# Kernel tuning notes

Hardware: AMD Instinct MI355X
Metric: run time of the kernel (lower is better)

The kernel has to match this reference:

```python
import jax, jax.numpy as jnp
import numpy as np

B, C, P, D = 4096, 1000, 10, 256
N = C * P            # total prototypes
E = 160000           # edges among prototypes
MARGIN = -0.1
LOSS_WEIGHT = 0.1
EPS = 1e-12          # F.normalize eps


def _gcn_conv(x, src, dst, deg_isqrt, w, b):
    # PyG GCNConv: symmetric-normalized aggregation with self-loops (added by caller)
    xw = x @ w                                   # [N, D]
    norm = deg_isqrt[src] * deg_isqrt[dst]       # [E+N]
    msg = norm[:, None] * xw[src]                # [E+N, D]
    out = jax.ops.segment_sum(msg, dst, num_segments=N)
    return out + b


def setup_inputs() -> dict:
    key = jax.random.key(0)
    ks = jax.random.split(key, 8)
    return {
        "hidden": jax.random.normal(ks[0], (B, D), jnp.float32),
        "labels": jax.random.randint(ks[1], (B,), 0, C),
        "edge_index": jax.random.randint(ks[2], (2, E), 0, N),
        "node_features": 0.02 * jax.random.normal(ks[3], (N, D), jnp.float32),
        "w1": jax.random.normal(ks[4], (D, D), jnp.float32) / np.sqrt(D),
        "b1": jnp.zeros((D,), jnp.float32),
        "w2": jax.random.normal(ks[5], (D, D), jnp.float32) / np.sqrt(D),
        "b2": jnp.zeros((D,), jnp.float32),
    }


def reference(hidden, labels, edge_index, node_features, w1, b1, w2, b2):
    # --- PrototypeGCN over the prototype graph (self-loops + sym norm) ---
    loops = jnp.arange(N, dtype=edge_index.dtype)
    src = jnp.concatenate([edge_index[0], loops])
    dst = jnp.concatenate([edge_index[1], loops])
    deg = jax.ops.segment_sum(jnp.ones_like(dst, jnp.float32), dst, num_segments=N)
    deg_isqrt = jnp.where(deg > 0, jax.lax.rsqrt(jnp.maximum(deg, 1.0)), 0.0)
    x = node_features
    x = jax.nn.relu(_gcn_conv(x, src, dst, deg_isqrt, w1, b1))
    x = jax.nn.relu(_gcn_conv(x, src, dst, deg_isqrt, w2, b2))

    # --- cosine similarity, per-class max over prototypes ---
    hidden_norm = hidden / jnp.maximum(jnp.linalg.norm(hidden, axis=1, keepdims=True), EPS)
    proto_norm = x / jnp.maximum(jnp.linalg.norm(x, axis=1, keepdims=True), EPS)
    sim = (1.0 + hidden_norm @ proto_norm.T) / 2.0          # [B, N]
    sim_pc = sim.reshape(B, C, P)
    output = sim_pc.max(axis=2)                              # [B, C]
    topk_idx = sim_pc.argmax(axis=2)                         # [B, C]

    # --- margin-masked cross entropy ---
    ar = jnp.arange(B)
    true_scores = output[ar, labels]
    pred_labels = output.argmax(axis=1)
    pred_scores = output.max(axis=1)
    mask = (true_scores - pred_scores) > MARGIN              # [B] bool
    cnt = mask.sum()
    per_ce = -jax.nn.log_softmax(output, axis=1)[ar, labels]
    ce_loss = jnp.sum(per_ce * mask) / jnp.maximum(cnt, 1).astype(per_ce.dtype)

    # dispersion = -mean(proto_norm @ proto_norm.T) = -||sum_i p_i||^2 / N^2
    s = proto_norm.sum(axis=0)
    dispersion_loss = -(s @ s) / (N * N)
    total_loss = jnp.where(cnt == 0, 0.0, ce_loss + LOSS_WEIGHT * dispersion_loss)

    # --- vectorized usage scatter (replaces Python double loop) ---
    pos_ids = labels * P + topk_idx[ar, labels]
    positive_usage = jnp.zeros((N,), jnp.float32).at[pos_ids].add(1.0)
    wrong = (pred_labels != labels).astype(jnp.float32)
    neg_ids = pred_labels * P + topk_idx[ar, pred_labels]
    negative_usage = jnp.zeros((N,), jnp.float32).at[neg_ids].add(wrong)

    return (output, total_loss, positive_usage, negative_usage)
```

## Files before the change

### kernel.cpp

```cpp
#include <hip/hip_runtime.h>
#include <math.h>

#define B_  4096
#define C_  1000
#define P_  10
#define D_  256
#define N_  10000
#define E_  160000

typedef __attribute__((ext_vector_type(8))) short short8;
typedef __attribute__((ext_vector_type(4))) float floatx4;

#define MFMA16(a, b, c) __builtin_amdgcn_mfma_f32_16x16x32_bf16((a), (b), (c), 0, 0, 0)

__device__ __forceinline__ float waveReduceSum(float v){
  #pragma unroll
  for (int o = 32; o > 0; o >>= 1) v += __shfl_xor(v, o);
  return v;
}
__device__ __forceinline__ unsigned short f2bf(float f){
  unsigned int u = __float_as_uint(f);
  unsigned int r = (u + 0x7FFFu + ((u >> 16) & 1u)) >> 16;
  return (unsigned short)r;
}
__device__ __forceinline__ float bf2f(unsigned short b){
  return __uint_as_float(((unsigned int)b) << 16);
}
__device__ __forceinline__ void split8(const float* __restrict__ p, short8& h8, short8& l8){
  float4 v0 = *(const float4*)p;
  float4 v1 = *(const float4*)(p + 4);
  float v[8] = {v0.x, v0.y, v0.z, v0.w, v1.x, v1.y, v1.z, v1.w};
  #pragma unroll
  for (int j = 0; j < 8; ++j){
    unsigned short h = f2bf(v[j]);
    h8[j] = (short)h;
    l8[j] = (short)f2bf(v[j] - bf2f(h));
  }
}

__global__ void k_scatter(const int* __restrict__ src, const int* __restrict__ dst,
                          int* __restrict__ cursor, int* __restrict__ csr_src){
  int e = blockIdx.x * 256 + threadIdx.x;
  if (e >= E_) return;
  int d = dst[e];
  int p = atomicAdd(&cursor[d], 1);
  p = (p < 63) ? p : 63;
  csr_src[d * 64 + p] = src[e];
}

__global__ void k_isq(const int* __restrict__ deg, float* __restrict__ isq){
  int n = blockIdx.x * 256 + threadIdx.x;
  if (n < N_) isq[n] = 1.0f / sqrtf((float)(deg[n] + 1));
}

__global__ void k_split_w(const float* __restrict__ w1, const float* __restrict__ w2,
                          unsigned short* __restrict__ w1h, unsigned short* __restrict__ w1l,
                          unsigned short* __restrict__ w2h, unsigned short* __restrict__ w2l){
  int b = blockIdx.x;
  int k = threadIdx.x;
  const float* w = (b < 256) ? w1 : w2;
  int n = b & 255;
  float x = w[(size_t)k * 256 + n];
  unsigned short h = f2bf(x);
  unsigned short l = f2bf(x - bf2f(h));
  if (b < 256){ w1h[(size_t)n * 256 + k] = h; w1l[(size_t)n * 256 + k] = l; }
  else        { w2h[(size_t)n * 256 + k] = h; w2l[(size_t)n * 256 + k] = l; }
}

__global__ __launch_bounds__(64) void k_gemm_mfma(
    const float* __restrict__ A,
    const unsigned short* __restrict__ Wh, const unsigned short* __restrict__ Wl,
    float* __restrict__ outp){
  int lane = threadIdx.x;
  int l15 = lane & 15, lq = lane >> 4;
  int rb = blockIdx.x * 64;
  int nb = blockIdx.y * 32;

  floatx4 acc[4][2];
  #pragma unroll
  for (int mt = 0; mt < 4; ++mt)
    #pragma unroll
    for (int nt = 0; nt < 2; ++nt) acc[mt][nt] = (floatx4){0.f,0.f,0.f,0.f};

  int arow[4];
  #pragma unroll
  for (int mt = 0; mt < 4; ++mt){
    int r = rb + mt * 16 + l15;
    arow[mt] = (r < N_) ? r : (N_ - 1);
  }
  for (int kc = 0; kc < 256; kc += 32){
    short8 ah[4], al[4], bh[2], bl[2];
    #pragma unroll
    for (int mt = 0; mt < 4; ++mt)
      split8(A + (size_t)arow[mt] * 256 + kc + lq * 8, ah[mt], al[mt]);
    #pragma unroll
    for (int nt = 0; nt < 2; ++nt){
      size_t o = (size_t)(nb + nt * 16 + l15) * 256 + kc + lq * 8;
      bh[nt] = *(const short8*)(Wh + o);
      bl[nt] = *(const short8*)(Wl + o);
    }
    #pragma unroll
    for (int nt = 0; nt < 2; ++nt)
      #pragma unroll
      for (int mt = 0; mt < 4; ++mt) acc[mt][nt] = MFMA16(al[mt], bh[nt], acc[mt][nt]);
    #pragma unroll
    for (int nt = 0; nt < 2; ++nt)
      #pragma unroll
      for (int mt = 0; mt < 4; ++mt) acc[mt][nt] = MFMA16(ah[mt], bl[nt], acc[mt][nt]);
    #pragma unroll
    for (int nt = 0; nt < 2; ++nt)
      #pragma unroll
      for (int mt = 0; mt < 4; ++mt) acc[mt][nt] = MFMA16(ah[mt], bh[nt], acc[mt][nt]);
  }
  #pragma unroll
  for (int mt = 0; mt < 4; ++mt)
    #pragma unroll
    for (int r = 0; r < 4; ++r){
      int row = rb + mt * 16 + lq * 4 + r;
      if (row < N_){
        #pragma unroll
        for (int nt = 0; nt < 2; ++nt)
          outp[(size_t)row * 256 + nb + nt * 16 + l15] = acc[mt][nt][r];
      }
    }
}

__global__ void k_agg_relu(const float* __restrict__ XW, const int* __restrict__ deg,
                           const int* __restrict__ csr_src, const float* __restrict__ isq,
                           const float* __restrict__ bias, float* __restrict__ X1){
  int n    = blockIdx.x * 4 + (threadIdx.x >> 6);
  int lane = threadIdx.x & 63;
  int c4   = lane * 4;
  int dg = deg[n]; dg = (dg < 64) ? dg : 64;
  int   esr = (lane < dg) ? csr_src[n * 64 + lane] : 0;
  float is  = isq[n];
  float en  = isq[esr] * is;
  float4 s = *(const float4*)(XW + (size_t)n * 256 + c4);
  float w = is * is;
  float4 a = make_float4(w * s.x, w * s.y, w * s.z, w * s.w);
  int i = 0;
  for (; i + 3 < dg; i += 4){
    int s0 = __shfl(esr, i),   s1 = __shfl(esr, i+1), s2 = __shfl(esr, i+2), s3 = __shfl(esr, i+3);
    float n0 = __shfl(en, i),  n1 = __shfl(en, i+1),  n2 = __shfl(en, i+2),  n3 = __shfl(en, i+3);
    float4 v0 = *(const float4*)(XW + (size_t)s0 * 256 + c4);
    float4 v1 = *(const float4*)(XW + (size_t)s1 * 256 + c4);
    float4 v2 = *(const float4*)(XW + (size_t)s2 * 256 + c4);
    float4 v3 = *(const float4*)(XW + (size_t)s3 * 256 + c4);
    a.x += n0*v0.x + n1*v1.x + n2*v2.x + n3*v3.x;
    a.y += n0*v0.y + n1*v1.y + n2*v2.y + n3*v3.y;
    a.z += n0*v0.z + n1*v1.z + n2*v2.z + n3*v3.z;
    a.w += n0*v0.w + n1*v1.w + n2*v2.w + n3*v3.w;
  }
  for (; i < dg; ++i){
    int s0 = __shfl(esr, i); float n0 = __shfl(en, i);
    float4 v0 = *(const float4*)(XW + (size_t)s0 * 256 + c4);
    a.x += n0 * v0.x; a.y += n0 * v0.y; a.z += n0 * v0.z; a.w += n0 * v0.w;
  }
  float4 b = *(const float4*)(bias + c4);
  float4 o;
  o.x = fmaxf(a.x + b.x, 0.f); o.y = fmaxf(a.y + b.y, 0.f);
  o.z = fmaxf(a.z + b.z, 0.f); o.w = fmaxf(a.w + b.w, 0.f);
  *(float4*)(X1 + (size_t)n * 256 + c4) = o;
}

__global__ void k_agg_norm_split(const float* __restrict__ XW, const int* __restrict__ deg,
                                 const int* __restrict__ csr_src, const float* __restrict__ isq,
                                 const float* __restrict__ bias,
                                 unsigned short* __restrict__ Ph, unsigned short* __restrict__ Pl){
  int n    = blockIdx.x * 4 + (threadIdx.x >> 6);
  int lane = threadIdx.x & 63;
  int c4   = lane * 4;
  int dg = deg[n]; dg = (dg < 64) ? dg : 64;
  int   esr = (lane < dg) ? csr_src[n * 64 + lane] : 0;
  float is  = isq[n];
  float en  = isq[esr] * is;
  float4 s = *(const float4*)(XW + (size_t)n * 256 + c4);
  float w = is * is;
  float4 a = make_float4(w * s.x, w * s.y, w * s.z, w * s.w);
  int i = 0;
  for (; i + 3 < dg; i += 4){
    int s0 = __shfl(esr, i),   s1 = __shfl(esr, i+1), s2 = __shfl(esr, i+2), s3 = __shfl(esr, i+3);
    float n0 = __shfl(en, i),  n1 = __shfl(en, i+1),  n2 = __shfl(en, i+2),  n3 = __shfl(en, i+3);
    float4 v0 = *(const float4*)(XW + (size_t)s0 * 256 + c4);
    float4 v1 = *(const float4*)(XW + (size_t)s1 * 256 + c4);
    float4 v2 = *(const float4*)(XW + (size_t)s2 * 256 + c4);
    float4 v3 = *(const float4*)(XW + (size_t)s3 * 256 + c4);
    a.x += n0*v0.x + n1*v1.x + n2*v2.x + n3*v3.x;
    a.y += n0*v0.y + n1*v1.y + n2*v2.y + n3*v3.y;
    a.z += n0*v0.z + n1*v1.z + n2*v2.z + n3*v3.z;
    a.w += n0*v0.w + n1*v1.w + n2*v2.w + n3*v3.w;
  }
  for (; i < dg; ++i){
    int s0 = __shfl(esr, i); float n0 = __shfl(en, i);
    float4 v0 = *(const float4*)(XW + (size_t)s0 * 256 + c4);
    a.x += n0 * v0.x; a.y += n0 * v0.y; a.z += n0 * v0.z; a.w += n0 * v0.w;
  }
  float4 b = *(const float4*)(bias + c4);
  float x0 = fmaxf(a.x + b.x, 0.f), x1 = fmaxf(a.y + b.y, 0.f);
  float x2 = fmaxf(a.z + b.z, 0.f), x3 = fmaxf(a.w + b.w, 0.f);
  float ss = x0*x0 + x1*x1 + x2*x2 + x3*x3;
  float tot = waveReduceSum(ss);
  float nrm = fmaxf(sqrtf(tot), 1e-12f);
  x0 /= nrm; x1 /= nrm; x2 /= nrm; x3 /= nrm;
  unsigned short h0 = f2bf(x0), h1 = f2bf(x1), h2 = f2bf(x2), h3 = f2bf(x3);
  ushort4 hv = make_ushort4(h0, h1, h2, h3);
  ushort4 lv = make_ushort4(f2bf(x0 - bf2f(h0)), f2bf(x1 - bf2f(h1)),
                            f2bf(x2 - bf2f(h2)), f2bf(x3 - bf2f(h3)));
  *(ushort4*)(Ph + (size_t)n * 256 + c4) = hv;
  *(ushort4*)(Pl + (size_t)n * 256 + c4) = lv;
}

__global__ void k_norm_split(const float* __restrict__ in,
                             unsigned short* __restrict__ hi,
                             unsigned short* __restrict__ lo){
  int r = blockIdx.x, t = threadIdx.x;
  float v = in[(size_t)r * 256 + t];
  float ss = waveReduceSum(v * v);
  __shared__ float red[4];
  int w = t >> 6;
  if ((t & 63) == 0) red[w] = ss;
  __syncthreads();
  float tot = red[0] + red[1] + red[2] + red[3];
  float nrm = fmaxf(sqrtf(tot), 1e-12f);
  float x = v / nrm;
  unsigned short h = f2bf(x);
  unsigned short l = f2bf(x - bf2f(h));
  hi[(size_t)r * 256 + t] = h;
  lo[(size_t)r * 256 + t] = l;
}

__global__ void k_colsum(const unsigned short* __restrict__ hi,
                         const unsigned short* __restrict__ lo,
                         float* __restrict__ s){
  int d = threadIdx.x;
  int r0 = blockIdx.x * 100;
  float acc = 0.f;
  for (int r = r0; r < r0 + 100; ++r)
    acc += bf2f(hi[(size_t)r * 256 + d]) + bf2f(lo[(size_t)r * 256 + d]);
  atomicAdd(&s[d], acc);
}

__global__ __launch_bounds__(256, 5) void k_sim_max(
    const unsigned short* __restrict__ HNh, const unsigned short* __restrict__ HNl,
    const unsigned short* __restrict__ PNh, const unsigned short* __restrict__ PNl,
    float* __restrict__ out, unsigned char* __restrict__ idxb){
  __shared__ __align__(16) char smem[25600];

  int tid  = threadIdx.x;
  int wid  = tid >> 6;
  int lane = tid & 63;
  int l15  = lane & 15, lq = lane >> 4;
  int rbw  = blockIdx.y * 128 + wid * 32;
  int cb80 = blockIdx.x * 80;

  floatx4 acc[2][5];
  #pragma unroll
  for (int mt = 0; mt < 2; ++mt)
    #pragma unroll
    for (int nt = 0; nt < 5; ++nt) acc[mt][nt] = (floatx4){0.f,0.f,0.f,0.f};

  const unsigned short* a0h = HNh + (size_t)(rbw + l15) * 256 + lq * 8;
  const unsigned short* a0l = HNl + (size_t)(rbw + l15) * 256 + lq * 8;

  auto stageB = [&](int kc, int pb){
    unsigned short* Bh = (unsigned short*)(smem + pb * 12800);
    unsigned short* Bl = Bh + 3200;
    #pragma unroll
    for (int f = tid; f < 640; f += 256){
      int dt = f >= 320;
      int f2 = f - (dt ? 320 : 0);
      int row = f2 >> 2, kq = f2 & 3;
      const unsigned short* gp = (dt ? PNl : PNh) + (size_t)(cb80 + row) * 256 + kc + kq * 8;
      uint4 v = *(const uint4*)gp;
      *(uint4*)((dt ? Bl : Bh) + row * 40 + kq * 8) = v;
    }
  };

  stageB(0, 0);
  short8 ah[2], al[2];
  #pragma unroll
  for (int mt = 0; mt < 2; ++mt){
    ah[mt] = *(const short8*)(a0h + (size_t)mt * 4096);
    al[mt] = *(const short8*)(a0l + (size_t)mt * 4096);
  }
  __syncthreads();

  int p = 0;
  for (int kc = 0; kc < 256; kc += 32){
    unsigned short* Bh = (unsigned short*)(smem + p * 12800);
    unsigned short* Bl = Bh + 3200;
    short8 ah2[2], al2[2];
    if (kc < 224){
      stageB(kc + 32, p ^ 1);
      #pragma unroll
      for (int mt = 0; mt < 2; ++mt){
        ah2[mt] = *(const short8*)(a0h + (size_t)mt * 4096 + kc + 32);
        al2[mt] = *(const short8*)(a0l + (size_t)mt * 4096 + kc + 32);
      }
    }
    #pragma unroll
    for (int nt2 = 0; nt2 < 4; nt2 += 2){
      int ro0 = ((nt2    ) * 16 + l15) * 40 + lq * 8;
      int ro1 = ((nt2 + 1) * 16 + l15) * 40 + lq * 8;
      short8 bh0 = *(const short8*)(Bh + ro0), bl0 = *(const short8*)(Bl + ro0);
      short8 bh1 = *(const short8*)(Bh + ro1), bl1 = *(const short8*)(Bl + ro1);
      acc[0][nt2]   = MFMA16(al[0], bh0, acc[0][nt2]);
      acc[1][nt2]   = MFMA16(al[1], bh0, acc[1][nt2]);
      acc[0][nt2+1] = MFMA16(al[0], bh1, acc[0][nt2+1]);
      acc[1][nt2+1] = MFMA16(al[1], bh1, acc[1][nt2+1]);
      acc[0][nt2]   = MFMA16(ah[0], bl0, acc[0][nt2]);
      acc[1][nt2]   = MFMA16(ah[1], bl0, acc[1][nt2]);
      acc[0][nt2+1] = MFMA16(ah[0], bl1, acc[0][nt2+1]);
      acc[1][nt2+1] = MFMA16(ah[1], bl1, acc[1][nt2+1]);
      acc[0][nt2]   = MFMA16(ah[0], bh0, acc[0][nt2]);
      acc[1][nt2]   = MFMA16(ah[1], bh0, acc[1][nt2]);
      acc[0][nt2+1] = MFMA16(ah[0], bh1, acc[0][nt2+1]);
      acc[1][nt2+1] = MFMA16(ah[1], bh1, acc[1][nt2+1]);
    }
    {
      int ro = (4 * 16 + l15) * 40 + lq * 8;
      short8 bh = *(const short8*)(Bh + ro), bl = *(const short8*)(Bl + ro);
      acc[0][4] = MFMA16(al[0], bh, acc[0][4]);
      acc[1][4] = MFMA16(al[1], bh, acc[1][4]);
      acc[0][4] = MFMA16(ah[0], bl, acc[0][4]);
      acc[1][4] = MFMA16(ah[1], bl, acc[1][4]);
      acc[0][4] = MFMA16(ah[0], bh, acc[0][4]);
      acc[1][4] = MFMA16(ah[1], bh, acc[1][4]);
    }
    ah[0] = ah2[0]; ah[1] = ah2[1];
    al[0] = al2[0]; al[1] = al2[1];
    __syncthreads();
    p ^= 1;
  }

  float* redw = (float*)smem + wid * 1296;
  #pragma unroll
  for (int mt = 0; mt < 2; ++mt){
    #pragma unroll
    for (int nt = 0; nt < 5; ++nt)
      #pragma unroll
      for (int r = 0; r < 4; ++r)
        redw[(lq * 4 + r) * 81 + nt * 16 + l15] = acc[mt][nt][r];
    int row = lane >> 2;
    int q   = lane & 3;
    const float* basep = redw + row * 81 + q * 20;
    float vs[2]; int is[2];
    #pragma unroll
    for (int cc = 0; cc < 2; ++cc){
      float m = 0.5f * (1.0f + basep[cc * 10]); int mi = 0;
      #pragma unroll
      for (int p2 = 1; p2 < 10; ++p2){
        float v = 0.5f * (1.0f + basep[cc * 10 + p2]);
        if (v > m){ m = v; mi = p2; }
      }
      vs[cc] = m; is[cc] = mi;
    }
    int grow = rbw + mt * 16 + row;
    int gcol = blockIdx.x * 8 + q * 2;
    *(float2*)(out + (size_t)grow * 1000 + gcol) = make_float2(vs[0], vs[1]);
    idxb[(size_t)grow * 1000 + gcol]     = (unsigned char)is[0];
    idxb[(size_t)grow * 1000 + gcol + 1] = (unsigned char)is[1];
  }
}

__global__ void k_row_pass(const float* __restrict__ out, const unsigned char* __restrict__ idxb,
                           const int* __restrict__ labels, int* __restrict__ cnt,
                           float* __restrict__ ce_sum, float* __restrict__ pos_usage,
                           float* __restrict__ neg_usage){
  int b = blockIdx.x * 4 + (threadIdx.x >> 6);
  int lane = threadIdx.x & 63;
  const float* row = out + (size_t)b * 1000;
  float m = -INFINITY, s = 0.f; int bi = 0x7fffffff;
  for (int c = lane; c < 1000; c += 64){
    float v = row[c];
    if (v > m){ s = s * expf(m - v) + 1.f; bi = c; m = v; }
    else       s += expf(v - m);
  }
  #pragma unroll
  for (int o = 32; o > 0; o >>= 1){
    float m2 = __shfl_xor(m, o);
    float s2 = __shfl_xor(s, o);
    int   b2 = __shfl_xor(bi, o);
    float M = fmaxf(m, m2);
    s = s * expf(m - M) + s2 * expf(m2 - M);
    if (m2 > m || (m2 == m && b2 < bi)) bi = b2;
    m = M;
  }
  if (lane == 0){
    int lab = labels[b];
    float true_score = row[lab];
    float per_ce = m + logf(s) - true_score;
    bool mask = (true_score - m) > -0.1f;
    if (mask){ atomicAdd(cnt, 1); atomicAdd(ce_sum, per_ce); }
    int pi = idxb[(size_t)b * 1000 + lab];
    atomicAdd(&pos_usage[lab * P_ + pi], 1.f);
    if (bi != lab){
      int ni = idxb[(size_t)b * 1000 + bi];
      atomicAdd(&neg_usage[bi * P_ + ni], 1.f);
    }
  }
}

__global__ void k_finalize(const float* __restrict__ s, const int* __restrict__ cnt,
                           const float* __restrict__ ce_sum, float* __restrict__ loss_out){
  int t = threadIdx.x;
  float v = s[t];
  float ss = waveReduceSum(v * v);
  __shared__ float red[4];
  if ((t & 63) == 0) red[t >> 6] = ss;
  __syncthreads();
  if (t == 0){
    float tot = red[0] + red[1] + red[2] + red[3];
    float disp = -tot / 1.0e8f;
    int c = *cnt;
    float total = (c == 0) ? 0.f
                : (*ce_sum / (float)(c < 1 ? 1 : c) + 0.1f * disp);
    *loss_out = total;
  }
}

extern "C" void kernel_launch(void* const* d_in, const int* in_sizes, int n_in,
                              void* d_out, int out_size, void* d_ws, size_t ws_size,
                              hipStream_t stream){
  const float* hidden = (const float*)d_in[0];
  const int*   labels = (const int*)  d_in[1];
  const int*   eidx   = (const int*)  d_in[2];
  const float* nodef  = (const float*)d_in[3];
  const float* w1     = (const float*)d_in[4];
  const float* b1     = (const float*)d_in[5];
  const float* w2     = (const float*)d_in[6];
  const float* b2     = (const float*)d_in[7];

  float* out       = (float*)d_out;
  float* loss_out  = out + (size_t)B_ * C_;
  float* pos_usage = loss_out + 1;
  float* neg_usage = pos_usage + N_;

  const int* srcp = eidx;
  const int* dstp = eidx + E_;

  char* base = (char*)d_ws;
  size_t off = 0;
  auto alloc = [&](size_t bytes) -> char* {
    char* p = base + off;
    off = (off + bytes + 255) & ~(size_t)255;
    return p;
  };
  int*   cursor  = (int*)  alloc((size_t)N_ * 4);
  float* svec    = (float*)alloc(256 * 4);
  int*   cnt     = (int*)  alloc(4);
  float* ce_sum  = (float*)alloc(4);
  size_t zero_bytes = off;
  float* deg_isqrt = (float*)alloc((size_t)N_ * 4);
  int*   csr_src   = (int*)  alloc((size_t)N_ * 64 * 4);
  float* XW        = (float*)alloc((size_t)N_ * 256 * 4);
  float* X1        = (float*)alloc((size_t)N_ * 256 * 4);
  unsigned short* Ph  = (unsigned short*)alloc((size_t)N_ * 256 * 2);
  unsigned short* Pl  = (unsigned short*)alloc((size_t)N_ * 256 * 2);
  unsigned short* W1h = (unsigned short*)alloc(256 * 256 * 2);
  unsigned short* W1l = (unsigned short*)alloc(256 * 256 * 2);
  unsigned short* W2h = (unsigned short*)alloc(256 * 256 * 2);
  unsigned short* W2l = (unsigned short*)alloc(256 * 256 * 2);
  unsigned short* HNh = (unsigned short*)alloc((size_t)B_ * 256 * 2);
  unsigned short* HNl = (unsigned short*)alloc((size_t)B_ * 256 * 2);
  unsigned char* idxb = (unsigned char*)alloc((size_t)B_ * C_);

  hipMemsetAsync(base, 0, zero_bytes, stream);
  hipMemsetAsync(loss_out, 0, (size_t)(1 + 2 * N_) * 4, stream);

  k_scatter<<<(E_ + 255) / 256, 256, 0, stream>>>(srcp, dstp, cursor, csr_src);
  k_isq<<<(N_ + 255) / 256, 256, 0, stream>>>(cursor, deg_isqrt);
  k_split_w<<<512, 256, 0, stream>>>(w1, w2, W1h, W1l, W2h, W2l);

  dim3 ggrid(157, 8);
  k_gemm_mfma<<<ggrid, 64, 0, stream>>>(nodef, W1h, W1l, XW);
  k_agg_relu<<<N_ / 4, 256, 0, stream>>>(XW, cursor, csr_src, deg_isqrt, b1, X1);
  k_gemm_mfma<<<ggrid, 64, 0, stream>>>(X1, W2h, W2l, XW);
  k_agg_norm_split<<<N_ / 4, 256, 0, stream>>>(XW, cursor, csr_src, deg_isqrt, b2, Ph, Pl);

  k_norm_split<<<B_, 256, 0, stream>>>(hidden, HNh, HNl);
  k_colsum<<<100, 256, 0, stream>>>(Ph, Pl, svec);

  dim3 sgrid(125, 32);
  k_sim_max<<<sgrid, 256, 0, stream>>>(HNh, HNl, Ph, Pl, out, idxb);

  k_row_pass<<<B_ / 4, 256, 0, stream>>>(out, idxb, labels, cnt, ce_sum, pos_usage, neg_usage);
  k_finalize<<<1, 256, 0, stream>>>(svec, cnt, ce_sum, loss_out);
}
```

Baseline: 382.4 us.

## Stage prototype tiles via direct global-to-LDS loads with XOR swizzle

Replaces the register round-trip staging of prototype hi/lo tiles with global_load_lds 16-byte direct loads into shared memory. The padded row stride of 40 is dropped in favour of a dense 32 stride with an XOR swizzle on the k-quarter to avoid bank conflicts. Shared memory shrinks and launch bounds drop from 5 to 4 blocks per SM, which may raise the register budget but lowers guaranteed occupancy. The intent is to cut VGPR pressure and load/store instructions in the main MFMA loop.

```diff
diff --git a/kernel.cpp b/kernel.cpp
--- a/kernel.cpp
+++ b/kernel.cpp
@@ -25,6 +25,10 @@
 }
 __device__ __forceinline__ float bf2f(unsigned short b){
   return __uint_as_float(((unsigned int)b) << 16);
+}
+__device__ __forceinline__ void gload_lds16(const void* g, void* l){
+  __builtin_amdgcn_global_load_lds((const __attribute__((address_space(1))) void*)g,
+                                   (__attribute__((address_space(3))) void*)l, 16, 0, 0);
 }
 __device__ __forceinline__ void split8(const float* __restrict__ p, short8& h8, short8& l8){
   float4 v0 = *(const float4*)p;
@@ -240,11 +244,11 @@
   atomicAdd(&s[d], acc);
 }
 
-__global__ __launch_bounds__(256, 5) void k_sim_max(
+__global__ __launch_bounds__(256, 4) void k_sim_max(
     const unsigned short* __restrict__ HNh, const unsigned short* __restrict__ HNl,
     const unsigned short* __restrict__ PNh, const unsigned short* __restrict__ PNl,
     float* __restrict__ out, unsigned char* __restrict__ idxb){
-  __shared__ __align__(16) char smem[25600];
+  __shared__ __align__(16) char smem[20736];
 
   int tid  = threadIdx.x;
   int wid  = tid >> 6;
@@ -253,6 +257,10 @@
   int rbw  = blockIdx.y * 128 + wid * 32;
   int cb80 = blockIdx.x * 80;
 
+  int swz  = (l15 >> 1) & 3;
+  int srow = lane >> 2;
+  int skq  = (lane & 3) ^ ((lane >> 3) & 3);
+
   floatx4 acc[2][5];
   #pragma unroll
   for (int mt = 0; mt < 2; ++mt)
@@ -262,21 +270,22 @@
   const unsigned short* a0h = HNh + (size_t)(rbw + l15) * 256 + lq * 8;
   const unsigned short* a0l = HNl + (size_t)(rbw + l15) * 256 + lq * 8;
 
-  auto stageB = [&](int kc, int pb){
-    unsigned short* Bh = (unsigned short*)(smem + pb * 12800);
-    unsigned short* Bl = Bh + 3200;
-    #pragma unroll
-    for (int f = tid; f < 640; f += 256){
-      int dt = f >= 320;
-      int f2 = f - (dt ? 320 : 0);
-      int row = f2 >> 2, kq = f2 & 3;
-      const unsigned short* gp = (dt ? PNl : PNh) + (size_t)(cb80 + row) * 256 + kc + kq * 8;
-      uint4 v = *(const uint4*)gp;
-      *(uint4*)((dt ? Bl : Bh) + row * 40 + kq * 8) = v;
-    }
+  auto stage1 = [&](int kc, int pb, int c){
+    int bsel = (c >= 5) ? 1 : 0;
+    int s = c - bsel * 5;
+    int row = s * 16 + srow;
+    const unsigned short* gp = (bsel ? PNl : PNh)
+        + (size_t)(cb80 + row) * 256 + kc + skq * 8;
+    char* lp = smem + pb * 10240 + bsel * 5120 + s * 1024;
+    gload_lds16(gp, lp);
   };
-
-  stageB(0, 0);
+  auto stageAll = [&](int kc, int pb){
+    stage1(kc, pb, wid);
+    stage1(kc, pb, wid + 4);
+    if (wid < 2) stage1(kc, pb, wid + 8);
+  };
+
+  stageAll(0, 0);
   short8 ah[2], al[2];
   #pragma unroll
   for (int mt = 0; mt < 2; ++mt){
@@ -287,11 +296,11 @@
 
   int p = 0;
   for (int kc = 0; kc < 256; kc += 32){
-    unsigned short* Bh = (unsigned short*)(smem + p * 12800);
-    unsigned short* Bl = Bh + 3200;
+    const unsigned short* Bh = (const unsigned short*)(smem + p * 10240);
+    const unsigned short* Bl = Bh + 2560;
     short8 ah2[2], al2[2];
     if (kc < 224){
-      stageB(kc + 32, p ^ 1);
+      stageAll(kc + 32, p ^ 1);
       #pragma unroll
       for (int mt = 0; mt < 2; ++mt){
         ah2[mt] = *(const short8*)(a0h + (size_t)mt * 4096 + kc + 32);
@@ -300,8 +309,8 @@
     }
     #pragma unroll
     for (int nt2 = 0; nt2 < 4; nt2 += 2){
-      int ro0 = ((nt2    ) * 16 + l15) * 40 + lq * 8;
-      int ro1 = ((nt2 + 1) * 16 + l15) * 40 + lq * 8;
+      int ro0 = ((nt2    ) * 16 + l15) * 32 + (lq ^ swz) * 8;
+      int ro1 = ((nt2 + 1) * 16 + l15) * 32 + (lq ^ swz) * 8;
       short8 bh0 = *(const short8*)(Bh + ro0), bl0 = *(const short8*)(Bl + ro0);
       short8 bh1 = *(const short8*)(Bh + ro1), bl1 = *(const short8*)(Bl + ro1);
       acc[0][nt2]   = MFMA16(al[0], bh0, acc[0][nt2]);
@@ -318,7 +327,7 @@
       acc[1][nt2+1] = MFMA16(ah[1], bh1, acc[1][nt2+1]);
     }
     {
-      int ro = (4 * 16 + l15) * 40 + lq * 8;
+      int ro = (4 * 16 + l15) * 32 + (lq ^ swz) * 8;
       short8 bh = *(const short8*)(Bh + ro), bl = *(const short8*)(Bl + ro);
       acc[0][4] = MFMA16(al[0], bh, acc[0][4]);
       acc[1][4] = MFMA16(al[1], bh, acc[1][4]);
```

Result: faster. 354.7 us (-7.3%).
